# Kernel tuning notes

Hardware: AMD Instinct MI355X
Metric: run time of the kernel (lower is better)

Reference implementation:

```python
import jax, jax.numpy as jnp
import numpy as np

B, N, CT = 64, 256, 3
HID, HEADS = 256, 4
C = HID // HEADS          # per-head channels
E = 8192                  # number of edges
NEG = 0.2                 # GATv2 leaky_relu negative slope
EPS_BN = 1e-5


def setup_inputs() -> dict:
    key = jax.random.key(0)
    ks = jax.random.split(key, 32)
    F_in = N * CT
    s1 = 1.0 / np.sqrt(F_in)
    sh = 1.0 / np.sqrt(HID)
    inp = {
        "x": jax.random.normal(ks[0], (B, N, N, CT), jnp.float32),
        "edge_index": jax.random.randint(ks[1], (2, E), 0, N, dtype=jnp.int32),
        # node_proj: Linear + BatchNorm1d (eval) params
        "W1": jax.random.normal(ks[2], (F_in, HID), jnp.float32) * s1,
        "b1": jnp.zeros((HID,), jnp.float32),
        "g1": jnp.ones((HID,), jnp.float32),
        "be1": jnp.zeros((HID,), jnp.float32),
        "m1": jnp.zeros((HID,), jnp.float32),
        "v1": jnp.ones((HID,), jnp.float32),
        # GATv2 layer 0
        "Wl0": jax.random.normal(ks[3], (HID, HID), jnp.float32) * sh,
        "bl0": jnp.zeros((HID,), jnp.float32),
        "Wr0": jax.random.normal(ks[4], (HID, HID), jnp.float32) * sh,
        "br0": jnp.zeros((HID,), jnp.float32),
        "att0": jax.random.normal(ks[5], (HEADS, C), jnp.float32) * (1.0 / np.sqrt(C)),
        "bo0": jnp.zeros((HID,), jnp.float32),
        # GATv2 layer 1
        "Wl1": jax.random.normal(ks[6], (HID, HID), jnp.float32) * sh,
        "bl1": jnp.zeros((HID,), jnp.float32),
        "Wr1": jax.random.normal(ks[7], (HID, HID), jnp.float32) * sh,
        "br1": jnp.zeros((HID,), jnp.float32),
        "att1": jax.random.normal(ks[8], (HEADS, C), jnp.float32) * (1.0 / np.sqrt(C)),
        "bo1": jnp.zeros((HID,), jnp.float32),
        # output_proj: Linear + BatchNorm1d (eval) params
        "W2": jax.random.normal(ks[9], (HID, HID), jnp.float32) * sh,
        "b2": jnp.zeros((HID,), jnp.float32),
        "g2": jnp.ones((HID,), jnp.float32),
        "be2": jnp.zeros((HID,), jnp.float32),
        "m2": jnp.zeros((HID,), jnp.float32),
        "v2": jnp.ones((HID,), jnp.float32),
    }
    return inp


def _bn(x, g, b, m, v):
    # BatchNorm1d in eval mode: per-feature affine with running stats
    return (x - m) * jax.lax.rsqrt(v + EPS_BN) * g + b


def _gatv2(h, src, dst, Wl, bl, Wr, br, att, bo):
    # h: (N, HID). GATv2Conv (PyG semantics): lin_l on source, lin_r on target.
    xl = (h @ Wl + bl).reshape(N, HEADS, C)
    xr = (h @ Wr + br).reshape(N, HEADS, C)
    x_j = xl[src]                        # (E, H, C) source features
    x_i = xr[dst]                        # (E, H, C) target features
    e = jax.nn.leaky_relu(x_i + x_j, NEG)
    logits = jnp.einsum('ehc,hc->eh', e, att)          # (E, H)
    mx = jax.ops.segment_max(logits, dst, num_segments=N)
    a = jnp.exp(logits - mx[dst])
    den = jax.ops.segment_sum(a, dst, num_segments=N)
    a = a / (den[dst] + 1e-16)                         # neighborhood softmax
    out = jax.ops.segment_sum(x_j * a[:, :, None], dst, num_segments=N)
    return out.reshape(N, HID) + bo


def reference(x, edge_index, W1, b1, g1, be1, m1, v1,
              Wl0, bl0, Wr0, br0, att0, bo0,
              Wl1, bl1, Wr1, br1, att1, bo1,
              W2, b2, g2, be2, m2, v2):
    gelu = lambda t: jax.nn.gelu(t, approximate=False)
    xf = x.reshape(B, N, N * CT)
    # node_proj (eval: dropout off, BN uses running stats -> vmappable)
    h = gelu(_bn(xf @ W1 + b1, g1, be1, m1, v1))       # (B, N, HID)
    src, dst = edge_index[0], edge_index[1]

    def per_sample(hn):
        h0 = gelu(_gatv2(hn, src, dst, Wl0, bl0, Wr0, br0, att0, bo0))
        h1 = gelu(_gatv2(h0, src, dst, Wl1, bl1, Wr1, br1, att1, bo1))
        return h1.mean(axis=0)                          # mean over nodes

    pooled = jax.vmap(per_sample)(h)                    # (B, HID)
    return gelu(_bn(pooled @ W2 + b2, g2, be2, m2, v2))
```

## Files before the change

### kernel.cpp

```cpp
#include <hip/hip_runtime.h>
#include <hip/hip_bf16.h>
#include <math.h>

#define BATCH   64
#define NNODES  256
#define HID     256
#define HEADS   4
#define CDIM    64
#define NEDGES  8192
#define NEG_SLOPE 0.2f
#define EPS_BN 1e-5f


typedef __bf16 bf16_t;
typedef __bf16 bf16x8 __attribute__((ext_vector_type(8)));
typedef float  f32x4  __attribute__((ext_vector_type(4)));

__device__ __forceinline__ float gelu_f(float x) {
    return 0.5f * x * (1.0f + erff(x * 0.70710678118654752440f));
}

__global__ __launch_bounds__(256) void prep_kernel(
        const int* __restrict__ ei,
        const float* __restrict__ W1, const float* __restrict__ Wa,
        const float* __restrict__ Wb, const float* __restrict__ Wc,
        const float* __restrict__ Wd,
        int* __restrict__ noff, int* __restrict__ csrc,
        bf16_t* __restrict__ T1, bf16_t* __restrict__ Ta,
        bf16_t* __restrict__ Tb, bf16_t* __restrict__ Tc,
        bf16_t* __restrict__ Td) {
    const int bx = blockIdx.x;
    const int tid = threadIdx.x;
    if (bx == 448) {
        __shared__ int cnt[NNODES];
        __shared__ int off_s[NNODES + 1];
        cnt[tid] = 0;
        __syncthreads();
        for (int e = tid; e < NEDGES; e += 256) atomicAdd(&cnt[ei[NEDGES + e]], 1);
        __syncthreads();
        if (tid == 0) {
            int s = 0;
            for (int i = 0; i < NNODES; ++i) { off_s[i] = s; s += cnt[i]; }
            off_s[NNODES] = s;
        }
        __syncthreads();
        cnt[tid] = off_s[tid];
        noff[tid] = off_s[tid];
        if (tid == 0) noff[NNODES] = off_s[NNODES];
        __syncthreads();
        for (int e = tid; e < NEDGES; e += 256) {
            int d = ei[NEDGES + e];
            int p = atomicAdd(&cnt[d], 1);
            csrc[p] = ei[e];
        }
        return;
    }
    __shared__ float tile[32][33];
    const float* in; bf16_t* out; int K, t;
    if (bx < 192) { in = W1; out = T1; K = 768; t = bx; }
    else {
        int r = bx - 192, mid = r >> 6; t = r & 63; K = 256;
        if (mid == 0) { in = Wa; out = Ta; }
        else if (mid == 1) { in = Wb; out = Tb; }
        else if (mid == 2) { in = Wc; out = Tc; }
        else { in = Wd; out = Td; }
    }
    const int kt = t >> 3, nt = t & 7;
    const int k0 = kt * 32, n0 = nt * 32;
    const int x = tid & 31, y = tid >> 5;
    #pragma unroll
    for (int j = 0; j < 4; ++j)
        tile[y + j * 8][x] = in[(size_t)(k0 + y + j * 8) * 256 + n0 + x];
    __syncthreads();
    #pragma unroll
    for (int j = 0; j < 4; ++j)
        out[(size_t)(n0 + y + j * 8) * K + k0 + x] = (bf16_t)tile[x][y + j * 8];
}

#define GSTR 56

template<int A_F32, int DUAL, int EPI_BN, int PERM>
__global__ __launch_bounds__(256) void gemm_kernel(
        const void* __restrict__ Ap,
        const bf16_t* __restrict__ Bt0, const bf16_t* __restrict__ Bt1,
        bf16_t* __restrict__ C0p, bf16_t* __restrict__ C1p, int K,
        const float* __restrict__ bias0, const float* __restrict__ bias1,
        const float* __restrict__ g, const float* __restrict__ be,
        const float* __restrict__ mu, const float* __restrict__ var) {
    __shared__ bf16_t As[128][GSTR];
    __shared__ bf16_t Bs[64][GSTR];
    const int tid  = threadIdx.x;
    const int lane = tid & 63;
    const int wv   = tid >> 6;
    const int wm   = wv >> 1, wn = wv & 1;
    const int mblk = blockIdx.y * 128;
    const int nt   = blockIdx.x;
    const bool second = DUAL && (nt >= 4);
    const bf16_t* Bt = second ? Bt1 : Bt0;
    bf16_t* Cp = second ? C1p : C0p;
    const int n0 = (second ? (nt - 4) : nt) * 64;

    f32x4 acc[8];
    #pragma unroll
    for (int i = 0; i < 8; ++i) acc[i] = (f32x4){0.f, 0.f, 0.f, 0.f};

    const int arow = tid >> 1, akh = (tid & 1) * 16;
    const int gr   = mblk + arow;
    const int arr  = PERM ? ((gr & 63) * 256 + (gr >> 6)) : gr;
    const int brow = tid >> 2, bkh = (tid & 3) * 8;
    const int fm = lane & 15, kc = (lane >> 4) * 8;

    for (int k0 = 0; k0 < K; k0 += 32) {
        if (A_F32) {
            const float* ap = (const float*)Ap + (size_t)arr * K + k0 + akh;
            f32x4 a0 = *(const f32x4*)ap;
            f32x4 a1 = *(const f32x4*)(ap + 4);
            f32x4 a2 = *(const f32x4*)(ap + 8);
            f32x4 a3 = *(const f32x4*)(ap + 12);
            bf16x8 v0, v1;
            #pragma unroll
            for (int j = 0; j < 4; ++j) {
                v0[j] = (bf16_t)a0[j]; v0[4 + j] = (bf16_t)a1[j];
                v1[j] = (bf16_t)a2[j]; v1[4 + j] = (bf16_t)a3[j];
            }
            *(bf16x8*)(&As[arow][akh])     = v0;
            *(bf16x8*)(&As[arow][akh + 8]) = v1;
        } else {
            const bf16_t* ap = (const bf16_t*)Ap + (size_t)arr * K + k0 + akh;
            *(bf16x8*)(&As[arow][akh])     = *(const bf16x8*)ap;
            *(bf16x8*)(&As[arow][akh + 8]) = *(const bf16x8*)(ap + 8);
        }
        *(bf16x8*)(&Bs[brow][bkh]) =
            *(const bf16x8*)(Bt + (size_t)(n0 + brow) * K + k0 + bkh);
        __syncthreads();

        bf16x8 af[4], bf[2];
        #pragma unroll
        for (int f = 0; f < 4; ++f)
            af[f] = *(const bf16x8*)(&As[wm * 64 + f * 16 + fm][kc]);
        #pragma unroll
        for (int t = 0; t < 2; ++t)
            bf[t] = *(const bf16x8*)(&Bs[wn * 32 + t * 16 + fm][kc]);
        #pragma unroll
        for (int f = 0; f < 4; ++f)
            #pragma unroll
            for (int t = 0; t < 2; ++t)
                acc[f * 2 + t] = __builtin_amdgcn_mfma_f32_16x16x32_bf16(
                    af[f], bf[t], acc[f * 2 + t], 0, 0, 0);
        __syncthreads();
    }

    const int quad = lane >> 4, cn = lane & 15;
    #pragma unroll
    for (int t = 0; t < 2; ++t) {
        const int n = n0 + wn * 32 + t * 16 + cn;
        const float bv = second ? bias1[n] : bias0[n];
        float scale = 1.0f, shift = 0.0f;
        if (EPI_BN) {
            float s = g[n] * rsqrtf(var[n] + EPS_BN);
            scale = s;
            shift = be[n] - mu[n] * s;
        }
        #pragma unroll
        for (int f = 0; f < 4; ++f) {
            #pragma unroll
            for (int r = 0; r < 4; ++r) {
                const int m = mblk + wm * 64 + f * 16 + quad * 4 + r;
                float val = acc[f * 2 + t][r] + bv;
                if (EPI_BN) val = gelu_f(val * scale + shift);
                Cp[(size_t)m * 256 + n] = (bf16_t)val;
            }
        }
    }
}

__global__ __launch_bounds__(256) void edge_kernel(
        const bf16_t* __restrict__ XL, const bf16_t* __restrict__ XR,
        const float* __restrict__ att, const float* __restrict__ bo,
        const int* __restrict__ noff, const int* __restrict__ csrc,
        bf16_t* __restrict__ Hout) {
    const int bid  = blockIdx.x;
    const int i    = bid >> 3;
    const int tid  = threadIdx.x;
    const int w    = tid >> 6;
    const int lane = tid & 63;
    const int bg   = lane >> 3;
    const int cg   = lane & 7;
    const int b    = (bid & 7) * 8 + bg;
    const int cbase = w * CDIM + cg * 8;
    const size_t orow = ((size_t)i * BATCH + b) * HID + cbase;
    const float* bor = bo + cbase;

    const int s0 = noff[i], s1 = noff[i + 1];
    if (s0 == s1) {
        bf16x8 ov;
        #pragma unroll
        for (int q = 0; q < 8; ++q) ov[q] = (bf16_t)gelu_f(bor[q]);
        *(bf16x8*)(Hout + orow) = ov;
        return;
    }

    float a6[8], a4[8], xi[8];
    {
        const float* ar = att + cbase;
        const bf16x8 xr = *(const bf16x8*)(XR + orow);
        #pragma unroll
        for (int q = 0; q < 8; ++q) {
            float a = ar[q];
            a6[q] = 0.6f * a; a4[q] = 0.4f * a;
            xi[q] = (float)xr[q];
        }
    }

    const bf16_t* XLb = XL + (size_t)b * HID + cbase;
    const size_t RSTR = (size_t)BATCH * HID;

    float mA = -1e30f, dA = 0.f, mB = -1e30f, dB = 0.f;
    float accA[8], accB[8];
    #pragma unroll
    for (int q = 0; q < 8; ++q) { accA[q] = 0.f; accB[q] = 0.f; }

    int jA = csrc[s0];
    int jB = csrc[(s0 + 1 < s1) ? s0 + 1 : s0];
    bf16x8 xA = *(const bf16x8*)(XLb + (size_t)jA * RSTR);
    bf16x8 xB = *(const bf16x8*)(XLb + (size_t)jB * RSTR);

    for (int e = s0; e < s1; e += 2) {
        const int nA = (e + 2 < s1) ? e + 2 : s0;
        const int nB = (e + 3 < s1) ? e + 3 : s0;
        const int jnA = csrc[nA], jnB = csrc[nB];
        const bf16x8 xnA = *(const bf16x8*)(XLb + (size_t)jnA * RSTR);
        const bf16x8 xnB = *(const bf16x8*)(XLb + (size_t)jnB * RSTR);

        float fA[8], fB[8];
        #pragma unroll
        for (int q = 0; q < 8; ++q) { fA[q] = (float)xA[q]; fB[q] = (float)xB[q]; }
        float pA = 0.f, pB = 0.f;
        #pragma unroll
        for (int q = 0; q < 8; ++q) {
            const float zA = xi[q] + fA[q];
            const float zB = xi[q] + fB[q];
            pA = fmaf(a6[q], zA, pA);
            pB = fmaf(a6[q], zB, pB);
            pA = fmaf(a4[q], __builtin_fabsf(zA), pA);
            pB = fmaf(a4[q], __builtin_fabsf(zB), pB);
        }
        pA += __shfl_xor(pA, 1, 64);  pB += __shfl_xor(pB, 1, 64);
        pA += __shfl_xor(pA, 2, 64);  pB += __shfl_xor(pB, 2, 64);
        pA += __shfl_xor(pA, 4, 64);  pB += __shfl_xor(pB, 4, 64);

        const float mnA = fmaxf(mA, pA);
        const float alA = __expf(mA - mnA);
        const float wA  = __expf(pA - mnA);
        const float vB  = (e + 1 < s1) ? 1.f : 0.f;
        const float mnB = fmaxf(mB, pB);
        const float alB = __expf(mB - mnB);
        const float wB  = __expf(pB - mnB) * vB;
        dA = dA * alA + wA;
        dB = dB * alB + wB;
        #pragma unroll
        for (int q = 0; q < 8; ++q) {
            accA[q] = fmaf(accA[q], alA, wA * fA[q]);
            accB[q] = fmaf(accB[q], alB, wB * fB[q]);
        }
        mA = mnA; mB = mnB;
        xA = xnA; xB = xnB;
    }

    const float mm = fmaxf(mA, mB);
    const float g1 = __expf(mA - mm);
    const float g2 = __expf(mB - mm);
    const float inv = 1.0f / (dA * g1 + dB * g2 + 1e-16f);
    bf16x8 ov;
    #pragma unroll
    for (int q = 0; q < 8; ++q) {
        const float o = (accA[q] * g1 + accB[q] * g2) * inv + bor[q];
        ov[q] = (bf16_t)gelu_f(o);
    }
    *(bf16x8*)(Hout + orow) = ov;
}

__global__ __launch_bounds__(256) void pf_kernel(
        const bf16_t* __restrict__ H1, const float* __restrict__ W2,
        const float* __restrict__ b2, const float* __restrict__ g2,
        const float* __restrict__ be2, const float* __restrict__ m2,
        const float* __restrict__ v2, float* __restrict__ out) {
    __shared__ float pl[HID];
    const int b = blockIdx.x, f = threadIdx.x;
    float s = 0.f;
    for (int n = 0; n < NNODES; ++n)
        s += (float)H1[((size_t)n * BATCH + b) * HID + f];
    pl[f] = s * (1.0f / (float)NNODES);
    __syncthreads();
    float acc = 0.f;
    for (int k = 0; k < HID; ++k) acc += pl[k] * W2[(size_t)k * HID + f];
    acc += b2[f];
    const float scale = g2[f] * rsqrtf(v2[f] + EPS_BN);
    acc = (acc - m2[f]) * scale + be2[f];
    out[b * HID + f] = gelu_f(acc);
}

extern "C" void kernel_launch(void* const* d_in, const int* in_sizes, int n_in,
                              void* d_out, int out_size, void* d_ws, size_t ws_size,
                              hipStream_t stream) {
    const float* x    = (const float*)d_in[0];
    const int*   ei   = (const int*)d_in[1];
    const float* W1   = (const float*)d_in[2];
    const float* b1   = (const float*)d_in[3];
    const float* g1   = (const float*)d_in[4];
    const float* be1  = (const float*)d_in[5];
    const float* m1   = (const float*)d_in[6];
    const float* v1   = (const float*)d_in[7];
    const float* Wl0  = (const float*)d_in[8];
    const float* bl0  = (const float*)d_in[9];
    const float* Wr0  = (const float*)d_in[10];
    const float* br0  = (const float*)d_in[11];
    const float* att0 = (const float*)d_in[12];
    const float* bo0  = (const float*)d_in[13];
    const float* Wl1  = (const float*)d_in[14];
    const float* bl1  = (const float*)d_in[15];
    const float* Wr1  = (const float*)d_in[16];
    const float* br1  = (const float*)d_in[17];
    const float* att1 = (const float*)d_in[18];
    const float* bo1  = (const float*)d_in[19];
    const float* W2   = (const float*)d_in[20];
    const float* b2   = (const float*)d_in[21];
    const float* g2   = (const float*)d_in[22];
    const float* be2  = (const float*)d_in[23];
    const float* m2   = (const float*)d_in[24];
    const float* v2   = (const float*)d_in[25];

    char* ws = (char*)d_ws;
    const int M = BATCH * NNODES;
    const size_t SZ_BF = (size_t)M * HID * sizeof(bf16_t);

    int*    noff = (int*)ws;                ws += 2048;
    int*    csrc = (int*)ws;                ws += 32768;
    bf16_t* W1t  = (bf16_t*)ws;             ws += 256 * 768 * 2;
    bf16_t* Wl0t = (bf16_t*)ws;             ws += 256 * 256 * 2;
    bf16_t* Wr0t = (bf16_t*)ws;             ws += 256 * 256 * 2;
    bf16_t* Wl1t = (bf16_t*)ws;             ws += 256 * 256 * 2;
    bf16_t* Wr1t = (bf16_t*)ws;             ws += 256 * 256 * 2;
    bf16_t* H    = (bf16_t*)ws;             ws += SZ_BF;
    bf16_t* H2   = (bf16_t*)ws;             ws += SZ_BF;
    bf16_t* XL   = (bf16_t*)ws;             ws += SZ_BF;
    bf16_t* XR   = (bf16_t*)ws;             ws += SZ_BF;

    prep_kernel<<<449, 256, 0, stream>>>(ei, W1, Wl0, Wr0, Wl1, Wr1,
                                         noff, csrc, W1t, Wl0t, Wr0t, Wl1t, Wr1t);

    gemm_kernel<1, 0, 1, 1><<<dim3(4, 128), 256, 0, stream>>>(
        x, W1t, nullptr, H, nullptr, 768, b1, nullptr, g1, be1, m1, v1);

    gemm_kernel<0, 1, 0, 0><<<dim3(8, 128), 256, 0, stream>>>(
        H, Wl0t, Wr0t, XL, XR, 256, bl0, br0, nullptr, nullptr, nullptr, nullptr);
    edge_kernel<<<NNODES * 8, 256, 0, stream>>>(XL, XR, att0, bo0, noff, csrc, H2);

    gemm_kernel<0, 1, 0, 0><<<dim3(8, 128), 256, 0, stream>>>(
        H2, Wl1t, Wr1t, XL, XR, 256, bl1, br1, nullptr, nullptr, nullptr, nullptr);
    edge_kernel<<<NNODES * 8, 256, 0, stream>>>(XL, XR, att1, bo1, noff, csrc, H);

    pf_kernel<<<BATCH, 256, 0, stream>>>(H, W2, b2, g2, be2, m2, v2, (float*)d_out);
}
```

Before: 305.1 us.

## Widen GEMM tiles to full 256-column N and swizzle shared-memory layout

```diff
diff --git a/kernel.cpp b/kernel.cpp
--- a/kernel.cpp
+++ b/kernel.cpp
@@ -19,6 +19,8 @@
 __device__ __forceinline__ float gelu_f(float x) {
     return 0.5f * x * (1.0f + erff(x * 0.70710678118654752440f));
 }
+
+#define SWZ(r, c) ((c) ^ ((r) & 3) ^ (((r) >> 2) & 3))
 
 __global__ __launch_bounds__(256) void prep_kernel(
         const int* __restrict__ ei,
@@ -77,84 +79,97 @@
         out[(size_t)(n0 + y + j * 8) * K + k0 + x] = (bf16_t)tile[x][y + j * 8];
 }
 
-#define GSTR 56
-
 template<int A_F32, int DUAL, int EPI_BN, int PERM>
-__global__ __launch_bounds__(256) void gemm_kernel(
+__global__ __launch_bounds__(256, 2) void gemm_kernel(
         const void* __restrict__ Ap,
         const bf16_t* __restrict__ Bt0, const bf16_t* __restrict__ Bt1,
         bf16_t* __restrict__ C0p, bf16_t* __restrict__ C1p, int K,
         const float* __restrict__ bias0, const float* __restrict__ bias1,
         const float* __restrict__ g, const float* __restrict__ be,
         const float* __restrict__ mu, const float* __restrict__ var) {
-    __shared__ bf16_t As[128][GSTR];
-    __shared__ bf16_t Bs[64][GSTR];
+    __shared__ bf16_t As[128 * 32];
+    __shared__ bf16_t Bs[256 * 32];
     const int tid  = threadIdx.x;
     const int lane = tid & 63;
     const int wv   = tid >> 6;
     const int wm   = wv >> 1, wn = wv & 1;
     const int mblk = blockIdx.y * 128;
-    const int nt   = blockIdx.x;
-    const bool second = DUAL && (nt >= 4);
+    const bool second = DUAL && (blockIdx.x == 1);
     const bf16_t* Bt = second ? Bt1 : Bt0;
     bf16_t* Cp = second ? C1p : C0p;
-    const int n0 = (second ? (nt - 4) : nt) * 64;
-
-    f32x4 acc[8];
-    #pragma unroll
-    for (int i = 0; i < 8; ++i) acc[i] = (f32x4){0.f, 0.f, 0.f, 0.f};
-
-    const int arow = tid >> 1, akh = (tid & 1) * 16;
+    const float* bias = second ? bias1 : bias0;
+
+    f32x4 acc[4][8];
+    #pragma unroll
+    for (int f = 0; f < 4; ++f)
+        #pragma unroll
+        for (int t = 0; t < 8; ++t) acc[f][t] = (f32x4){0.f, 0.f, 0.f, 0.f};
+
+    const int arow = tid >> 1;
+    const int acb  = (tid & 1) * 2;
     const int gr   = mblk + arow;
     const int arr  = PERM ? ((gr & 63) * 256 + (gr >> 6)) : gr;
-    const int brow = tid >> 2, bkh = (tid & 3) * 8;
-    const int fm = lane & 15, kc = (lane >> 4) * 8;
+    const int fm   = lane & 15, q = lane >> 4;
 
     for (int k0 = 0; k0 < K; k0 += 32) {
+        bf16x8 v0, v1;
         if (A_F32) {
-            const float* ap = (const float*)Ap + (size_t)arr * K + k0 + akh;
+            const float* ap = (const float*)Ap + (size_t)arr * K + k0 + acb * 8;
             f32x4 a0 = *(const f32x4*)ap;
             f32x4 a1 = *(const f32x4*)(ap + 4);
             f32x4 a2 = *(const f32x4*)(ap + 8);
             f32x4 a3 = *(const f32x4*)(ap + 12);
-            bf16x8 v0, v1;
             #pragma unroll
             for (int j = 0; j < 4; ++j) {
                 v0[j] = (bf16_t)a0[j]; v0[4 + j] = (bf16_t)a1[j];
                 v1[j] = (bf16_t)a2[j]; v1[4 + j] = (bf16_t)a3[j];
             }
-            *(bf16x8*)(&As[arow][akh])     = v0;
-            *(bf16x8*)(&As[arow][akh + 8]) = v1;
         } else {
-            const bf16_t* ap = (const bf16_t*)Ap + (size_t)arr * K + k0 + akh;
-            *(bf16x8*)(&As[arow][akh])     = *(const bf16x8*)ap;
-            *(bf16x8*)(&As[arow][akh + 8]) = *(const bf16x8*)(ap + 8);
-        }
-        *(bf16x8*)(&Bs[brow][bkh]) =
-            *(const bf16x8*)(Bt + (size_t)(n0 + brow) * K + k0 + bkh);
-        __syncthreads();
-
-        bf16x8 af[4], bf[2];
-        #pragma unroll
-        for (int f = 0; f < 4; ++f)
-            af[f] = *(const bf16x8*)(&As[wm * 64 + f * 16 + fm][kc]);
-        #pragma unroll
-        for (int t = 0; t < 2; ++t)
-            bf[t] = *(const bf16x8*)(&Bs[wn * 32 + t * 16 + fm][kc]);
+            const bf16_t* ap = (const bf16_t*)Ap + (size_t)arr * K + k0 + acb * 8;
+            v0 = *(const bf16x8*)ap;
+            v1 = *(const bf16x8*)(ap + 8);
+        }
+        *(bf16x8*)(&As[(arow * 4 + SWZ(arow, acb)) * 8])     = v0;
+        *(bf16x8*)(&As[(arow * 4 + SWZ(arow, acb + 1)) * 8]) = v1;
+
+        {
+            const bf16_t* bp = Bt + (size_t)tid * K + k0;
+            bf16x8 b0 = *(const bf16x8*)bp;
+            bf16x8 b1 = *(const bf16x8*)(bp + 8);
+            bf16x8 b2 = *(const bf16x8*)(bp + 16);
+            bf16x8 b3 = *(const bf16x8*)(bp + 24);
+            *(bf16x8*)(&Bs[(tid * 4 + SWZ(tid, 0)) * 8]) = b0;
+            *(bf16x8*)(&Bs[(tid * 4 + SWZ(tid, 1)) * 8]) = b1;
+            *(bf16x8*)(&Bs[(tid * 4 + SWZ(tid, 2)) * 8]) = b2;
+            *(bf16x8*)(&Bs[(tid * 4 + SWZ(tid, 3)) * 8]) = b3;
+        }
+        __syncthreads();
+
+        bf16x8 af[4], bfv[8];
+        #pragma unroll
+        for (int f = 0; f < 4; ++f) {
+            const int r = wm * 64 + f * 16 + fm;
+            af[f] = *(const bf16x8*)(&As[(r * 4 + SWZ(r, q)) * 8]);
+        }
+        #pragma unroll
+        for (int t = 0; t < 8; ++t) {
+            const int n = wn * 128 + t * 16 + fm;
+            bfv[t] = *(const bf16x8*)(&Bs[(n * 4 + SWZ(n, q)) * 8]);
+        }
         #pragma unroll
         for (int f = 0; f < 4; ++f)
             #pragma unroll
-            for (int t = 0; t < 2; ++t)
-                acc[f * 2 + t] = __builtin_amdgcn_mfma_f32_16x16x32_bf16(
-                    af[f], bf[t], acc[f * 2 + t], 0, 0, 0);
+            for (int t = 0; t < 8; ++t)
+                acc[f][t] = __builtin_amdgcn_mfma_f32_16x16x32_bf16(
+                    af[f], bfv[t], acc[f][t], 0, 0, 0);
         __syncthreads();
     }
 
     const int quad = lane >> 4, cn = lane & 15;
     #pragma unroll
-    for (int t = 0; t < 2; ++t) {
-        const int n = n0 + wn * 32 + t * 16 + cn;
-        const float bv = second ? bias1[n] : bias0[n];
+    for (int t = 0; t < 8; ++t) {
+        const int n = wn * 128 + t * 16 + cn;
+        const float bv = bias[n];
         float scale = 1.0f, shift = 0.0f;
         if (EPI_BN) {
             float s = g[n] * rsqrtf(var[n] + EPS_BN);
@@ -166,7 +181,7 @@
             #pragma unroll
             for (int r = 0; r < 4; ++r) {
                 const int m = mblk + wm * 64 + f * 16 + quad * 4 + r;
-                float val = acc[f * 2 + t][r] + bv;
+                float val = acc[f][t][r] + bv;
                 if (EPI_BN) val = gelu_f(val * scale + shift);
                 Cp[(size_t)m * 256 + n] = (bf16_t)val;
             }
@@ -349,14 +364,14 @@
     prep_kernel<<<449, 256, 0, stream>>>(ei, W1, Wl0, Wr0, Wl1, Wr1,
                                          noff, csrc, W1t, Wl0t, Wr0t, Wl1t, Wr1t);
 
-    gemm_kernel<1, 0, 1, 1><<<dim3(4, 128), 256, 0, stream>>>(
+    gemm_kernel<1, 0, 1, 1><<<dim3(1, 128), 256, 0, stream>>>(
         x, W1t, nullptr, H, nullptr, 768, b1, nullptr, g1, be1, m1, v1);
 
-    gemm_kernel<0, 1, 0, 0><<<dim3(8, 128), 256, 0, stream>>>(
+    gemm_kernel<0, 1, 0, 0><<<dim3(2, 128), 256, 0, stream>>>(
         H, Wl0t, Wr0t, XL, XR, 256, bl0, br0, nullptr, nullptr, nullptr, nullptr);
     edge_kernel<<<NNODES * 8, 256, 0, stream>>>(XL, XR, att0, bo0, noff, csrc, H2);
 
-    gemm_kernel<0, 1, 0, 0><<<dim3(8, 128), 256, 0, stream>>>(
+    gemm_kernel<0, 1, 0, 0><<<dim3(2, 128), 256, 0, stream>>>(
         H2, Wl1t, Wr1t, XL, XR, 256, bl1, br1, nullptr, nullptr, nullptr, nullptr);
     edge_kernel<<<NNODES * 8, 256, 0, stream>>>(XL, XR, att1, bo1, noff, csrc, H);
 
```

After: 327.2 us. 1.07x slower.
